# Optimization experiments

Hardware: AMD Instinct MI355X
Metric: run time of the kernel (lower is better)

## Reference

```python
import jax, jax.numpy as jnp
import numpy as np

N_NODES = 100000
N_EDGES = 600000
HIDDEN = 128
N_LAYERS = 4
ALPHA = 0.1


def setup_inputs() -> dict:
    key = jax.random.key(0)
    ks = jax.random.split(key, 8)
    x = jax.random.normal(ks[0], (N_NODES, HIDDEN), dtype=jnp.float32)
    src = jax.random.randint(ks[1], (N_EDGES,), 0, N_NODES, dtype=jnp.int32)
    dst = jax.random.randint(ks[2], (N_EDGES,), 0, N_NODES, dtype=jnp.int32)
    w = jax.random.uniform(ks[3], (N_EDGES,), dtype=jnp.float32)
    # per-layer GCN linear weights (stored as [in, out]) and biases
    scale = 1.0 / np.sqrt(HIDDEN)
    Ws = jax.random.normal(ks[4], (N_LAYERS, HIDDEN, HIDDEN), dtype=jnp.float32) * scale
    bs = jnp.zeros((N_LAYERS, HIDDEN), dtype=jnp.float32)
    # energy heads: Linear(hidden, 1) for each of num_layers+1 taps
    We = jax.random.normal(ks[5], (N_LAYERS + 1, HIDDEN), dtype=jnp.float32) * scale
    be = jnp.zeros((N_LAYERS + 1,), dtype=jnp.float32)
    # GPR combination weights: alpha*(1-alpha)^k, last = (1-alpha)^L
    t = ALPHA * (1.0 - ALPHA) ** np.arange(N_LAYERS + 1)
    t[-1] = (1.0 - ALPHA) ** N_LAYERS
    temp = jnp.asarray(t, dtype=jnp.float32)
    return {"x": x, "src": src, "dst": dst, "w": w,
            "Ws": Ws, "bs": bs, "We": We, "be": be, "temp": temp}


def reference(x, src, dst, w, Ws, bs, We, be, temp):
    # eval mode: both dropouts are identity
    def gcn_conv(h, W, b):
        h = h @ W + b                      # [N, d] dense projection
        msg = h[src] * w[:, None]          # gather + edge-weight scale [E, d]
        return jax.ops.segment_sum(msg, dst, num_segments=N_NODES)  # scatter-sum

    energy = (x @ We[0] + be[0])[:, None] * temp[0]   # [N, 1]
    for i in range(N_LAYERS):
        x = gcn_conv(x, Ws[i], bs[i])
        x = jax.nn.leaky_relu(x, negative_slope=0.01)
        energy = energy + (x @ We[i + 1] + be[i + 1])[:, None] * temp[i + 1]
    return energy, x
```

## Files before the change

### kernel.cpp

```cpp
#include <hip/hip_runtime.h>
#include <hip/hip_bf16.h>

#define N_NODES 100000
#define N_EDGES 600000
#define HIDDEN 128
#define N_LAYERS 4
#define MPAD 100096
#define CPAD 16

#define TAP0_BLOCKS ((N_NODES * 16) / 256)
#define CNT_BLOCKS ((N_EDGES + 255) / 256)
#define PREPW_BLOCKS ((N_LAYERS * HIDDEN * HIDDEN + 255) / 256)
#define GEMM_BLOCKS (MPAD / 64)

typedef short bf16x8 __attribute__((ext_vector_type(8)));
typedef float f32x4 __attribute__((ext_vector_type(4)));
typedef float f32x8 __attribute__((ext_vector_type(8)));

__device__ inline ushort f2bf(float f) {
    __hip_bfloat16 h = __float2bfloat16(f);
    return *reinterpret_cast<ushort*>(&h);
}

__device__ inline float bfhi(uint u) { return __uint_as_float(u << 16); }
__device__ inline float bflo(uint u) { return __uint_as_float(u & 0xffff0000u); }

#define FMA8(U, P) { float wk = __int_as_float(P.y); \
    a[0] += bfhi(U.x) * wk; a[1] += bflo(U.x) * wk; \
    a[2] += bfhi(U.y) * wk; a[3] += bflo(U.y) * wk; \
    a[4] += bfhi(U.z) * wk; a[5] += bflo(U.z) * wk; \
    a[6] += bfhi(U.w) * wk; a[7] += bflo(U.w) * wk; }

__device__ __forceinline__ void gather_agg(const char* __restrict__ hrow,
                                           const int2* __restrict__ epack,
                                           int j0, int j1, int cb, float* a) {
    int j = j0;
    for (; j + 4 <= j1; j += 4) {
        int2 p0 = epack[j], p1 = epack[j + 1], p2 = epack[j + 2], p3 = epack[j + 3];
        uint4 u0 = *(const uint4*)(hrow + (size_t)p0.x * 256 + cb);
        uint4 u1 = *(const uint4*)(hrow + (size_t)p1.x * 256 + cb);
        uint4 u2 = *(const uint4*)(hrow + (size_t)p2.x * 256 + cb);
        uint4 u3 = *(const uint4*)(hrow + (size_t)p3.x * 256 + cb);
        FMA8(u0, p0); FMA8(u1, p1); FMA8(u2, p2); FMA8(u3, p3);
    }
    if (j + 2 <= j1) {
        int2 p0 = epack[j], p1 = epack[j + 1];
        uint4 u0 = *(const uint4*)(hrow + (size_t)p0.x * 256 + cb);
        uint4 u1 = *(const uint4*)(hrow + (size_t)p1.x * 256 + cb);
        FMA8(u0, p0); FMA8(u1, p1);
        j += 2;
    }
    if (j < j1) {
        int2 p0 = epack[j];
        uint4 u0 = *(const uint4*)(hrow + (size_t)p0.x * 256 + cb);
        FMA8(u0, p0);
    }
}

__global__ void prologue(const float* __restrict__ x, const float* __restrict__ We,
                         const float* __restrict__ be, const float* __restrict__ temp,
                         float* __restrict__ energy, uint* __restrict__ xb,
                         const int* __restrict__ dst, int* __restrict__ cnt,
                         int* __restrict__ eslot,
                         const float* __restrict__ Ws, ushort* __restrict__ whi,
                         ushort* __restrict__ wlo) {
    int b = blockIdx.x;
    if (b < TAP0_BLOCKS) {
        int gtid = b * 256 + threadIdx.x;
        int n = gtid >> 4, l16 = gtid & 15;
        f32x8 v = *(const f32x8*)(x + (size_t)n * HIDDEN + l16 * 8);
        uint4 packed;
        packed.x = (uint)f2bf(v[0]) | ((uint)f2bf(v[1]) << 16);
        packed.y = (uint)f2bf(v[2]) | ((uint)f2bf(v[3]) << 16);
        packed.z = (uint)f2bf(v[4]) | ((uint)f2bf(v[5]) << 16);
        packed.w = (uint)f2bf(v[6]) | ((uint)f2bf(v[7]) << 16);
        ((uint4*)(xb + (size_t)n * 64))[l16] = packed;
        f32x8 we = *(const f32x8*)(We + l16 * 8);
        float dot = v[0] * we[0] + v[1] * we[1] + v[2] * we[2] + v[3] * we[3]
                  + v[4] * we[4] + v[5] * we[5] + v[6] * we[6] + v[7] * we[7];
        #pragma unroll
        for (int off = 8; off > 0; off >>= 1) dot += __shfl_xor(dot, off);
        if (l16 == 0) energy[n] = (dot + be[0]) * temp[0];
    } else if (b < TAP0_BLOCKS + CNT_BLOCKS) {
        int e = (b - TAP0_BLOCKS) * 256 + threadIdx.x;
        if (e < N_EDGES)
            eslot[e] = atomicAdd(&cnt[(size_t)dst[e] * CPAD], 1);
    } else {
        int idx = (b - TAP0_BLOCKS - CNT_BLOCKS) * 256 + threadIdx.x;
        if (idx < N_LAYERS * HIDDEN * HIDDEN) {
            int l = idx >> 14;
            int r = idx & 16383;
            int c = r >> 7, k = r & 127;
            float v = Ws[(l << 14) + k * HIDDEN + c];
            ushort hi = f2bf(v);
            float hif = __uint_as_float(((uint)hi) << 16);
            whi[idx] = hi;
            wlo[idx] = f2bf(v - hif);
        }
    }
}

__global__ void scan1(const int* __restrict__ cnt, int* __restrict__ excl,
                      int* __restrict__ bsums, int n) {
    __shared__ int lds[8];
    int t = threadIdx.x;
    int base = blockIdx.x * 1024 + t * 4;
    int v0 = (base + 0 < n) ? cnt[(size_t)(base + 0) * CPAD] : 0;
    int v1 = (base + 1 < n) ? cnt[(size_t)(base + 1) * CPAD] : 0;
    int v2 = (base + 2 < n) ? cnt[(size_t)(base + 2) * CPAD] : 0;
    int v3 = (base + 3 < n) ? cnt[(size_t)(base + 3) * CPAD] : 0;
    int tsum = v0 + v1 + v2 + v3;
    int lane = t & 63, wv = t >> 6;
    int s = tsum;
    #pragma unroll
    for (int off = 1; off < 64; off <<= 1) {
        int u = __shfl_up(s, off);
        if (lane >= off) s += u;
    }
    if (lane == 63) lds[wv] = s;
    __syncthreads();
    if (t == 0) {
        int a = 0;
        #pragma unroll
        for (int i = 0; i < 4; ++i) { int bb = lds[i]; lds[i] = a; a += bb; }
        lds[4] = a;
    }
    __syncthreads();
    int excl_t = (s - tsum) + lds[wv];
    if (base + 0 < n) excl[base + 0] = excl_t;
    if (base + 1 < n) excl[base + 1] = excl_t + v0;
    if (base + 2 < n) excl[base + 2] = excl_t + v0 + v1;
    if (base + 3 < n) excl[base + 3] = excl_t + v0 + v1 + v2;
    if (t == 0) bsums[blockIdx.x] = lds[4];
}

__global__ void scan23(const int* __restrict__ excl, const int* __restrict__ bsums,
                       int* __restrict__ rowptr, int n, int nb) {
    __shared__ int bp[128];
    int t = threadIdx.x;
    if (t < nb) bp[t] = bsums[t];
    __syncthreads();
    if (t == 0) {
        int a = 0;
        for (int i = 0; i < nb; ++i) { int v = bp[i]; bp[i] = a; a += v; }
    }
    __syncthreads();
    int i = blockIdx.x * blockDim.x + t;
    if (i < n) rowptr[i] = excl[i] + bp[i >> 10];
    else if (i == n) rowptr[n] = N_EDGES;
}

__global__ __launch_bounds__(256) void fill_gemm0(
    const int* __restrict__ src, const int* __restrict__ dst,
    const float* __restrict__ w, const int* __restrict__ rowptr,
    const int* __restrict__ eslot, int2* __restrict__ epack,
    const uint* __restrict__ xb,
    const ushort* __restrict__ whi, const ushort* __restrict__ wlo,
    const float* __restrict__ b, ushort* __restrict__ h) {
    int t = threadIdx.x;
    int bm = blockIdx.x % 5;
    if (bm >= 2) {
        int fid = (blockIdx.x / 5) * 3 + (bm - 2);
        int e = fid * 256 + t;
        if (e < N_EDGES) {
            int d = dst[e];
            epack[rowptr[d] + eslot[e]] = make_int2(src[e], __float_as_int(w[e]));
        }
        return;
    }
    int gid = (blockIdx.x / 5) * 2 + bm;

    __shared__ uint4 sx4[1024];
    char* sxb = (char*)sx4;
    int lane = t & 63, wv = t >> 6;
    int l15 = lane & 15, l4 = lane >> 4;
    int row0 = gid * 64;
    int c0 = wv * 32;

    bf16x8 Ah[2][4], Al[2][4];
    #pragma unroll
    for (int m = 0; m < 2; ++m) {
        int c = c0 + m * 16 + l15;
        #pragma unroll
        for (int s = 0; s < 4; ++s) {
            int off = c * HIDDEN + s * 32 + l4 * 8;
            Ah[m][s] = *(const bf16x8*)(whi + off);
            Al[m][s] = *(const bf16x8*)(wlo + off);
        }
    }

    #pragma unroll
    for (int j = 0; j < 4; ++j) {
        int c = j * 256 + t;
        int row = c >> 4;
        int colb = (c & 15) * 16;
        int grow = row0 + row;
        if (grow >= N_NODES) grow = N_NODES - 1;
        uint4 v = *(const uint4*)((const char*)xb + (size_t)grow * 256 + colb);
        *(uint4*)(sxb + row * 256 + (colb ^ ((row & 7) << 4))) = v;
    }
    __syncthreads();

    f32x4 acc[2][4];
    #pragma unroll
    for (int m = 0; m < 2; ++m)
        #pragma unroll
        for (int n = 0; n < 4; ++n)
            acc[m][n] = f32x4{0.f, 0.f, 0.f, 0.f};

    #pragma unroll
    for (int n = 0; n < 4; ++n) {
        int row = n * 16 + l15;
        int rsw = (row & 7) << 4;
        #pragma unroll
        for (int s = 0; s < 4; ++s) {
            bf16x8 bh = *(const bf16x8*)(sxb + row * 256 + ((s * 64 + l4 * 16) ^ rsw));
            #pragma unroll
            for (int m = 0; m < 2; ++m) {
                acc[m][n] = __builtin_amdgcn_mfma_f32_16x16x32_bf16(Ah[m][s], bh, acc[m][n], 0, 0, 0);
                acc[m][n] = __builtin_amdgcn_mfma_f32_16x16x32_bf16(Al[m][s], bh, acc[m][n], 0, 0, 0);
            }
        }
    }

    #pragma unroll
    for (int m = 0; m < 2; ++m) {
        f32x4 bias = *(const f32x4*)(b + c0 + m * 16 + l4 * 4);
        #pragma unroll
        for (int n = 0; n < 4; ++n) {
            int node = row0 + n * 16 + l15;
            f32x4 r = acc[m][n] + bias;
            uint2 packed;
            packed.x = (uint)f2bf(r[0]) | ((uint)f2bf(r[1]) << 16);
            packed.y = (uint)f2bf(r[2]) | ((uint)f2bf(r[3]) << 16);
            *(uint2*)(h + (size_t)node * HIDDEN + c0 + m * 16 + l4 * 4) = packed;
        }
    }
}

__global__ __launch_bounds__(512) void agg_gemm(
    const ushort* __restrict__ hprev, const int* __restrict__ rowptr,
    const int2* __restrict__ epack,
    const float* __restrict__ We_l, const float* __restrict__ be_l,
    const float* __restrict__ temp_l, float* __restrict__ energy,
    const ushort* __restrict__ whi, const ushort* __restrict__ wlo,
    const float* __restrict__ b, ushort* __restrict__ hnext) {
    __shared__ uint4 sx4[1024];
    char* sxb = (char*)sx4;
    int t = threadIdx.x;
    int row0 = blockIdx.x * 64;
    int g = t >> 4, l16 = t & 15;
    int cb = l16 * 16;
    const char* hrow = (const char*)hprev;

    #pragma unroll 1
    for (int p = 0; p < 2; ++p) {
        int r = p * 32 + g;
        int n = row0 + r;
        float a[8] = {0.f, 0.f, 0.f, 0.f, 0.f, 0.f, 0.f, 0.f};
        if (n < N_NODES) {
            int j0 = rowptr[n], j1 = rowptr[n + 1];
            gather_agg(hrow, epack, j0, j1, cb, a);
            #pragma unroll
            for (int q = 0; q < 8; ++q) a[q] = a[q] > 0.f ? a[q] : 0.01f * a[q];
            const float* wer = We_l + l16 * 8;
            float4 we0 = *(const float4*)(wer + 0);
            float4 we1 = *(const float4*)(wer + 4);
            float dot = a[0] * we0.x + a[1] * we0.y + a[2] * we0.z + a[3] * we0.w
                      + a[4] * we1.x + a[5] * we1.y + a[6] * we1.z + a[7] * we1.w;
            #pragma unroll
            for (int off = 8; off > 0; off >>= 1) dot += __shfl_xor(dot, off);
            if (l16 == 0) energy[n] += (dot + be_l[0]) * temp_l[0];
        }
        uint4 packed;
        packed.x = (uint)f2bf(a[0]) | ((uint)f2bf(a[1]) << 16);
        packed.y = (uint)f2bf(a[2]) | ((uint)f2bf(a[3]) << 16);
        packed.z = (uint)f2bf(a[4]) | ((uint)f2bf(a[5]) << 16);
        packed.w = (uint)f2bf(a[6]) | ((uint)f2bf(a[7]) << 16);
        *(uint4*)(sxb + r * 256 + (cb ^ ((r & 7) << 4))) = packed;
    }

    int lane = t & 63, wv = t >> 6;
    int l15 = lane & 15, l4 = lane >> 4;
    int c0 = wv * 16;
    bf16x8 Ah[4], Al[4];
    #pragma unroll
    for (int s = 0; s < 4; ++s) {
        int off = (c0 + l15) * HIDDEN + s * 32 + l4 * 8;
        Ah[s] = *(const bf16x8*)(whi + off);
        Al[s] = *(const bf16x8*)(wlo + off);
    }
    __syncthreads();

    f32x4 acc[4];
    #pragma unroll
    for (int n = 0; n < 4; ++n) acc[n] = f32x4{0.f, 0.f, 0.f, 0.f};

    #pragma unroll
    for (int n = 0; n < 4; ++n) {
        int row = n * 16 + l15;
        int rsw = (row & 7) << 4;
        #pragma unroll
        for (int s = 0; s < 4; ++s) {
            bf16x8 bh = *(const bf16x8*)(sxb + row * 256 + ((s * 64 + l4 * 16) ^ rsw));
            acc[n] = __builtin_amdgcn_mfma_f32_16x16x32_bf16(Ah[s], bh, acc[n], 0, 0, 0);
            acc[n] = __builtin_amdgcn_mfma_f32_16x16x32_bf16(Al[s], bh, acc[n], 0, 0, 0);
        }
    }

    f32x4 bias = *(const f32x4*)(b + c0 + l4 * 4);
    #pragma unroll
    for (int n = 0; n < 4; ++n) {
        int node = row0 + n * 16 + l15;
        f32x4 r = acc[n] + bias;
        uint2 packed;
        packed.x = (uint)f2bf(r[0]) | ((uint)f2bf(r[1]) << 16);
        packed.y = (uint)f2bf(r[2]) | ((uint)f2bf(r[3]) << 16);
        *(uint2*)(hnext + (size_t)node * HIDDEN + c0 + l4 * 4) = packed;
    }
}

__global__ void agg_final(const ushort* __restrict__ h, const int* __restrict__ rowptr,
                          const int2* __restrict__ epack,
                          const float* __restrict__ We_l, const float* __restrict__ be_l,
                          const float* __restrict__ temp_l,
                          float* __restrict__ xout, float* __restrict__ energy) {
    int gtid = blockIdx.x * blockDim.x + threadIdx.x;
    int n = gtid >> 4;
    int l16 = gtid & 15;
    if (n >= N_NODES) return;
    int j0 = rowptr[n], j1 = rowptr[n + 1];
    int cb = l16 * 16;
    float a[8] = {0.f, 0.f, 0.f, 0.f, 0.f, 0.f, 0.f, 0.f};
    gather_agg((const char*)h, epack, j0, j1, cb, a);
    #pragma unroll
    for (int q = 0; q < 8; ++q) a[q] = a[q] > 0.f ? a[q] : 0.01f * a[q];

    float* orow = xout + (size_t)n * HIDDEN + l16 * 8;
    *(float4*)(orow + 0) = float4{a[0], a[1], a[2], a[3]};
    *(float4*)(orow + 4) = float4{a[4], a[5], a[6], a[7]};

    const float* wer = We_l + l16 * 8;
    float4 we0 = *(const float4*)(wer + 0);
    float4 we1 = *(const float4*)(wer + 4);
    float dot = a[0] * we0.x + a[1] * we0.y + a[2] * we0.z + a[3] * we0.w
              + a[4] * we1.x + a[5] * we1.y + a[6] * we1.z + a[7] * we1.w;
    #pragma unroll
    for (int off = 8; off > 0; off >>= 1) dot += __shfl_xor(dot, off);
    if (l16 == 0) energy[n] += (dot + be_l[0]) * temp_l[0];
}

extern "C" void kernel_launch(void* const* d_in, const int* in_sizes, int n_in,
                              void* d_out, int out_size, void* d_ws, size_t ws_size,
                              hipStream_t stream) {
    const float* x    = (const float*)d_in[0];
    const int*   src  = (const int*)d_in[1];
    const int*   dst  = (const int*)d_in[2];
    const float* w    = (const float*)d_in[3];
    const float* Ws   = (const float*)d_in[4];
    const float* bs   = (const float*)d_in[5];
    const float* We   = (const float*)d_in[6];
    const float* be   = (const float*)d_in[7];
    const float* temp = (const float*)d_in[8];

    float* energy = (float*)d_out;
    float* xout   = (float*)d_out + N_NODES;
    uint* xb = (uint*)xout;

    ushort* h0     = (ushort*)d_ws;
    ushort* h1     = h0 + (size_t)MPAD * HIDDEN;
    int2*   epack  = (int2*)(h1 + (size_t)MPAD * HIDDEN);
    int*    cnt    = (int*)(epack + N_EDGES);
    int*    eslot  = cnt + (size_t)N_NODES * CPAD;
    int*    excl   = eslot + N_EDGES;
    int*    bsums  = excl + N_NODES;
    int*    rowptr = bsums + 128;
    ushort* whi    = (ushort*)(rowptr + N_NODES + 4);
    ushort* wlo    = whi + N_LAYERS * HIDDEN * HIDDEN;

    hipMemsetAsync(cnt, 0, (size_t)N_NODES * CPAD * sizeof(int), stream);

    prologue<<<TAP0_BLOCKS + CNT_BLOCKS + PREPW_BLOCKS, 256, 0, stream>>>(
        x, We, be, temp, energy, xb, dst, cnt, eslot, Ws, whi, wlo);

    int nblk = (N_NODES + 1023) / 1024;
    scan1<<<nblk, 256, 0, stream>>>(cnt, excl, bsums, N_NODES);
    scan23<<<(N_NODES + 1 + 255) / 256, 256, 0, stream>>>(excl, bsums, rowptr, N_NODES, nblk);

    fill_gemm0<<<GEMM_BLOCKS + CNT_BLOCKS, 256, 0, stream>>>(
        src, dst, w, rowptr, eslot, epack, xb, whi, wlo, bs, h0);

    agg_gemm<<<GEMM_BLOCKS, 512, 0, stream>>>(
        h0, rowptr, epack, We + 1 * HIDDEN, be + 1, temp + 1, energy,
        whi + 1 * HIDDEN * HIDDEN, wlo + 1 * HIDDEN * HIDDEN, bs + 1 * HIDDEN, h1);
    agg_gemm<<<GEMM_BLOCKS, 512, 0, stream>>>(
        h1, rowptr, epack, We + 2 * HIDDEN, be + 2, temp + 2, energy,
        whi + 2 * HIDDEN * HIDDEN, wlo + 2 * HIDDEN * HIDDEN, bs + 2 * HIDDEN, h0);
    agg_gemm<<<GEMM_BLOCKS, 512, 0, stream>>>(
        h0, rowptr, epack, We + 3 * HIDDEN, be + 3, temp + 3, energy,
        whi + 3 * HIDDEN * HIDDEN, wlo + 3 * HIDDEN * HIDDEN, bs + 3 * HIDDEN, h1);

    agg_final<<<(N_NODES * 16 + 255) / 256, 256, 0, stream>>>(
        h1, rowptr, epack, We + 4 * HIDDEN, be + 4, temp + 4, xout, energy);
}
```

Before: 265.9 us.

## Make agg_gemm a persistent kernel with atomic ticket tile scheduling

agg_gemm now launches a fixed 1024 blocks that repeatedly grab 64-row tiles through an atomic ticket counter. Before, it launched one block per tile. The weight fragments, bias and energy-head weights are loaded once per block instead of once per tile. Dynamic tile assignment should also balance the irregular per-node degree work. The cost is an extra atomic and barrier per tile, ticket counters reset in scan23, and fewer resident waves to hide gather latency.

```diff
diff --git a/kernel.cpp b/kernel.cpp
--- a/kernel.cpp
+++ b/kernel.cpp
@@ -12,6 +12,7 @@
 #define CNT_BLOCKS ((N_EDGES + 255) / 256)
 #define PREPW_BLOCKS ((N_LAYERS * HIDDEN * HIDDEN + 255) / 256)
 #define GEMM_BLOCKS (MPAD / 64)
+#define PERS_BLOCKS 1024
 
 typedef short bf16x8 __attribute__((ext_vector_type(8)));
 typedef float f32x4 __attribute__((ext_vector_type(4)));
@@ -135,9 +136,11 @@
 }
 
 __global__ void scan23(const int* __restrict__ excl, const int* __restrict__ bsums,
-                       int* __restrict__ rowptr, int n, int nb) {
+                       int* __restrict__ rowptr, int n, int nb,
+                       int* __restrict__ tickets) {
     __shared__ int bp[128];
     int t = threadIdx.x;
+    if (blockIdx.x == 0 && t < 8) tickets[t] = 0;
     if (t < nb) bp[t] = bsums[t];
     __syncthreads();
     if (t == 0) {
@@ -244,45 +247,20 @@
     const float* __restrict__ We_l, const float* __restrict__ be_l,
     const float* __restrict__ temp_l, float* __restrict__ energy,
     const ushort* __restrict__ whi, const ushort* __restrict__ wlo,
-    const float* __restrict__ b, ushort* __restrict__ hnext) {
+    const float* __restrict__ b, ushort* __restrict__ hnext,
+    int* __restrict__ ticket) {
     __shared__ uint4 sx4[1024];
+    __shared__ int s_tile;
     char* sxb = (char*)sx4;
     int t = threadIdx.x;
-    int row0 = blockIdx.x * 64;
     int g = t >> 4, l16 = t & 15;
     int cb = l16 * 16;
     const char* hrow = (const char*)hprev;
 
-    #pragma unroll 1
-    for (int p = 0; p < 2; ++p) {
-        int r = p * 32 + g;
-        int n = row0 + r;
-        float a[8] = {0.f, 0.f, 0.f, 0.f, 0.f, 0.f, 0.f, 0.f};
-        if (n < N_NODES) {
-            int j0 = rowptr[n], j1 = rowptr[n + 1];
-            gather_agg(hrow, epack, j0, j1, cb, a);
-            #pragma unroll
-            for (int q = 0; q < 8; ++q) a[q] = a[q] > 0.f ? a[q] : 0.01f * a[q];
-            const float* wer = We_l + l16 * 8;
-            float4 we0 = *(const float4*)(wer + 0);
-            float4 we1 = *(const float4*)(wer + 4);
-            float dot = a[0] * we0.x + a[1] * we0.y + a[2] * we0.z + a[3] * we0.w
-                      + a[4] * we1.x + a[5] * we1.y + a[6] * we1.z + a[7] * we1.w;
-            #pragma unroll
-            for (int off = 8; off > 0; off >>= 1) dot += __shfl_xor(dot, off);
-            if (l16 == 0) energy[n] += (dot + be_l[0]) * temp_l[0];
-        }
-        uint4 packed;
-        packed.x = (uint)f2bf(a[0]) | ((uint)f2bf(a[1]) << 16);
-        packed.y = (uint)f2bf(a[2]) | ((uint)f2bf(a[3]) << 16);
-        packed.z = (uint)f2bf(a[4]) | ((uint)f2bf(a[5]) << 16);
-        packed.w = (uint)f2bf(a[6]) | ((uint)f2bf(a[7]) << 16);
-        *(uint4*)(sxb + r * 256 + (cb ^ ((r & 7) << 4))) = packed;
-    }
-
     int lane = t & 63, wv = t >> 6;
     int l15 = lane & 15, l4 = lane >> 4;
     int c0 = wv * 16;
+
     bf16x8 Ah[4], Al[4];
     #pragma unroll
     for (int s = 0; s < 4; ++s) {
@@ -290,33 +268,71 @@
         Ah[s] = *(const bf16x8*)(whi + off);
         Al[s] = *(const bf16x8*)(wlo + off);
     }
-    __syncthreads();
-
-    f32x4 acc[4];
-    #pragma unroll
-    for (int n = 0; n < 4; ++n) acc[n] = f32x4{0.f, 0.f, 0.f, 0.f};
-
-    #pragma unroll
-    for (int n = 0; n < 4; ++n) {
-        int row = n * 16 + l15;
-        int rsw = (row & 7) << 4;
-        #pragma unroll
-        for (int s = 0; s < 4; ++s) {
-            bf16x8 bh = *(const bf16x8*)(sxb + row * 256 + ((s * 64 + l4 * 16) ^ rsw));
-            acc[n] = __builtin_amdgcn_mfma_f32_16x16x32_bf16(Ah[s], bh, acc[n], 0, 0, 0);
-            acc[n] = __builtin_amdgcn_mfma_f32_16x16x32_bf16(Al[s], bh, acc[n], 0, 0, 0);
-        }
-    }
-
-    f32x4 bias = *(const f32x4*)(b + c0 + l4 * 4);
-    #pragma unroll
-    for (int n = 0; n < 4; ++n) {
-        int node = row0 + n * 16 + l15;
-        f32x4 r = acc[n] + bias;
-        uint2 packed;
-        packed.x = (uint)f2bf(r[0]) | ((uint)f2bf(r[1]) << 16);
-        packed.y = (uint)f2bf(r[2]) | ((uint)f2bf(r[3]) << 16);
-        *(uint2*)(hnext + (size_t)node * HIDDEN + c0 + l4 * 4) = packed;
+    float4 bias = *(const float4*)(b + c0 + l4 * 4);
+    const float* wer = We_l + l16 * 8;
+    float4 we0 = *(const float4*)(wer + 0);
+    float4 we1 = *(const float4*)(wer + 4);
+    float be_v = be_l[0], tp_v = temp_l[0];
+
+    for (;;) {
+        if (t == 0) s_tile = atomicAdd(ticket, 1);
+        __syncthreads();
+        int tile = s_tile;
+        if (tile >= GEMM_BLOCKS) break;
+        int row0 = tile * 64;
+
+        #pragma unroll 1
+        for (int p = 0; p < 2; ++p) {
+            int r = p * 32 + g;
+            int n = row0 + r;
+            float a[8] = {0.f, 0.f, 0.f, 0.f, 0.f, 0.f, 0.f, 0.f};
+            if (n < N_NODES) {
+                int j0 = rowptr[n], j1 = rowptr[n + 1];
+                gather_agg(hrow, epack, j0, j1, cb, a);
+                #pragma unroll
+                for (int q = 0; q < 8; ++q) a[q] = a[q] > 0.f ? a[q] : 0.01f * a[q];
+                float dot = a[0] * we0.x + a[1] * we0.y + a[2] * we0.z + a[3] * we0.w
+                          + a[4] * we1.x + a[5] * we1.y + a[6] * we1.z + a[7] * we1.w;
+                #pragma unroll
+                for (int off = 8; off > 0; off >>= 1) dot += __shfl_xor(dot, off);
+                if (l16 == 0) energy[n] += (dot + be_v) * tp_v;
+            }
+            uint4 packed;
+            packed.x = (uint)f2bf(a[0]) | ((uint)f2bf(a[1]) << 16);
+            packed.y = (uint)f2bf(a[2]) | ((uint)f2bf(a[3]) << 16);
+            packed.z = (uint)f2bf(a[4]) | ((uint)f2bf(a[5]) << 16);
+            packed.w = (uint)f2bf(a[6]) | ((uint)f2bf(a[7]) << 16);
+            *(uint4*)(sxb + r * 256 + (cb ^ ((r & 7) << 4))) = packed;
+        }
+        __syncthreads();
+
+        f32x4 acc[4];
+        #pragma unroll
+        for (int n = 0; n < 4; ++n) acc[n] = f32x4{0.f, 0.f, 0.f, 0.f};
+
+        #pragma unroll
+        for (int n = 0; n < 4; ++n) {
+            int row = n * 16 + l15;
+            int rsw = (row & 7) << 4;
+            #pragma unroll
+            for (int s = 0; s < 4; ++s) {
+                bf16x8 bh = *(const bf16x8*)(sxb + row * 256 + ((s * 64 + l4 * 16) ^ rsw));
+                acc[n] = __builtin_amdgcn_mfma_f32_16x16x32_bf16(Ah[s], bh, acc[n], 0, 0, 0);
+                acc[n] = __builtin_amdgcn_mfma_f32_16x16x32_bf16(Al[s], bh, acc[n], 0, 0, 0);
+            }
+        }
+
+        #pragma unroll
+        for (int n = 0; n < 4; ++n) {
+            int node = row0 + n * 16 + l15;
+            f32x4 r = acc[n];
+            r[0] += bias.x; r[1] += bias.y; r[2] += bias.z; r[3] += bias.w;
+            uint2 packed;
+            packed.x = (uint)f2bf(r[0]) | ((uint)f2bf(r[1]) << 16);
+            packed.y = (uint)f2bf(r[2]) | ((uint)f2bf(r[3]) << 16);
+            *(uint2*)(hnext + (size_t)node * HIDDEN + c0 + l4 * 4) = packed;
+        }
+        __syncthreads();
     }
 }
 
@@ -375,7 +391,8 @@
     int*    excl   = eslot + N_EDGES;
     int*    bsums  = excl + N_NODES;
     int*    rowptr = bsums + 128;
-    ushort* whi    = (ushort*)(rowptr + N_NODES + 4);
+    int*    tickets= rowptr + N_NODES + 4;
+    ushort* whi    = (ushort*)(tickets + 8);
     ushort* wlo    = whi + N_LAYERS * HIDDEN * HIDDEN;
 
     hipMemsetAsync(cnt, 0, (size_t)N_NODES * CPAD * sizeof(int), stream);
@@ -385,20 +402,24 @@
 
     int nblk = (N_NODES + 1023) / 1024;
     scan1<<<nblk, 256, 0, stream>>>(cnt, excl, bsums, N_NODES);
-    scan23<<<(N_NODES + 1 + 255) / 256, 256, 0, stream>>>(excl, bsums, rowptr, N_NODES, nblk);
+    scan23<<<(N_NODES + 1 + 255) / 256, 256, 0, stream>>>(excl, bsums, rowptr,
+                                                          N_NODES, nblk, tickets);
 
     fill_gemm0<<<GEMM_BLOCKS + CNT_BLOCKS, 256, 0, stream>>>(
         src, dst, w, rowptr, eslot, epack, xb, whi, wlo, bs, h0);
 
-    agg_gemm<<<GEMM_BLOCKS, 512, 0, stream>>>(
+    agg_gemm<<<PERS_BLOCKS, 512, 0, stream>>>(
         h0, rowptr, epack, We + 1 * HIDDEN, be + 1, temp + 1, energy,
-        whi + 1 * HIDDEN * HIDDEN, wlo + 1 * HIDDEN * HIDDEN, bs + 1 * HIDDEN, h1);
-    agg_gemm<<<GEMM_BLOCKS, 512, 0, stream>>>(
+        whi + 1 * HIDDEN * HIDDEN, wlo + 1 * HIDDEN * HIDDEN, bs + 1 * HIDDEN, h1,
+        tickets + 0);
+    agg_gemm<<<PERS_BLOCKS, 512, 0, stream>>>(
         h1, rowptr, epack, We + 2 * HIDDEN, be + 2, temp + 2, energy,
-        whi + 2 * HIDDEN * HIDDEN, wlo + 2 * HIDDEN * HIDDEN, bs + 2 * HIDDEN, h0);
-    agg_gemm<<<GEMM_BLOCKS, 512, 0, stream>>>(
+        whi + 2 * HIDDEN * HIDDEN, wlo + 2 * HIDDEN * HIDDEN, bs + 2 * HIDDEN, h0,
+        tickets + 1);
+    agg_gemm<<<PERS_BLOCKS, 512, 0, stream>>>(
         h0, rowptr, epack, We + 3 * HIDDEN, be + 3, temp + 3, energy,
-        whi + 3 * HIDDEN * HIDDEN, wlo + 3 * HIDDEN * HIDDEN, bs + 3 * HIDDEN, h1);
+        whi + 3 * HIDDEN * HIDDEN, wlo + 3 * HIDDEN * HIDDEN, bs + 3 * HIDDEN, h1,
+        tickets + 2);
 
     agg_final<<<(N_NODES * 16 + 255) / 256, 256, 0, stream>>>(
         h1, rowptr, epack, We + 4 * HIDDEN, be + 4, temp + 4, xout, energy);
```

Measured after the change: 273.6 us. 2.9% more time.
